# Performance work log

Hardware: AMD Instinct MI355X
Metric: run time of the kernel (lower is better)

Reference implementation:

```python
import jax, jax.numpy as jnp
import numpy as np

THR = 1.0
ALPHA = 5.0
C = 0.4
TAU_U = 20.0
DT = 1.0

def slayer(x):
    # SE-adlif SLAYER surrogate: c*alpha / (2*exp(alpha*|x|))
    return C * ALPHA / (2.0 * jnp.exp(jnp.abs(x) * ALPHA))

def setup_inputs() -> dict:
    key = jax.random.key(0)
    k1, k2, k3 = jax.random.split(key, 3)
    B, T, IN, OUT = 64, 1000, 512, 512
    x = jax.random.normal(k1, (B, T, IN), dtype=jnp.float32)
    lim = 1.0 / np.sqrt(IN)
    weight = jax.random.uniform(k2, (OUT, IN), minval=-lim, maxval=lim, dtype=jnp.float32)
    bias = jnp.zeros((OUT,), jnp.float32)
    # orthogonal init for recurrent weights
    recurrent = jnp.linalg.qr(jax.random.normal(k3, (OUT, OUT), dtype=jnp.float32))[0].astype(jnp.float32)
    # fixed tau trainer: decay = exp(-dt/tau)
    decay = jnp.full((OUT,), np.exp(-DT / TAU_U), dtype=jnp.float32)
    return {"input_tensor": x, "weight": weight, "bias": bias, "recurrent": recurrent, "decay": decay}

def reference(input_tensor, weight, bias, recurrent, decay):
    B = input_tensor.shape[0]
    OUT = weight.shape[0]
    sg = jax.lax.stop_gradient
    # precompute input-driven current for all timesteps: [B, T, OUT]
    cur = jnp.einsum('bti,oi->bto', input_tensor, weight) + bias
    v0 = jnp.zeros((B, OUT), jnp.float32)
    z0 = jnp.zeros((B, OUT), jnp.float32)

    def step(carry, c_t):
        v_tm1, z_tm1 = carry
        v_tm1 = v_tm1 * (1.0 - sg(z_tm1))  # detached reset
        soma = c_t + z_tm1 @ recurrent.T
        v_t = decay * v_tm1 + (1.0 - decay) * soma
        v_thr = v_t - THR
        hv = jnp.where(v_thr >= 0, 1.0, 0.0).astype(v_thr.dtype)
        # straight-through: value = heaviside, grad = SLAYER surrogate
        z_t = sg(hv) + (v_thr - sg(v_thr)) * sg(slayer(v_thr))
        return (v_t, z_t), (v_t, z_t)

    _, (vs, zs) = jax.lax.scan(step, (v0, z0), jnp.swapaxes(cur, 0, 1))
    vs = jnp.swapaxes(vs, 0, 1)  # [B, T, OUT]
    zs = jnp.swapaxes(zs, 0, 1)
    v_full = jnp.concatenate([v0[:, None], vs], axis=1)  # [B, T+1, OUT]
    z_full = jnp.concatenate([z0[:, None], zs], axis=1)
    states = jnp.stack([v_full, z_full], axis=0)  # [2, B, T+1, OUT]
    outputs = zs  # [B, T, OUT]
    return outputs, states
```

## Files before the change

kernel.cpp:

```cpp
#include <hip/hip_runtime.h>

#define SV_OFF 32768000
#define SZ_OFF 65568768

typedef __attribute__((ext_vector_type(8))) short bf16x8;
typedef __attribute__((ext_vector_type(4))) float f32x4;

__device__ __forceinline__ unsigned short f2bf(float f) {
  union { float f; unsigned u; } x; x.f = f;
  unsigned r = x.u + 0x7fffu + ((x.u >> 16) & 1u);
  return (unsigned short)(r >> 16);
}

__device__ __forceinline__ void gl_lds16(const void* g, void* l) {
  __builtin_amdgcn_global_load_lds(
      (const __attribute__((address_space(1))) unsigned int*)g,
      (__attribute__((address_space(3))) unsigned int*)l, 16, 0, 0);
}

__global__ __launch_bounds__(256) void prep(const float* __restrict__ W,
                                            unsigned short* __restrict__ Wb,
                                            int* __restrict__ flags) {
  const int idx = blockIdx.x * 256 + threadIdx.x;
  if (idx < 512 * 512) Wb[idx] = f2bf(W[idx]);
  if (idx < 64) flags[idx] = 0;
}

__global__ __launch_bounds__(256) void cvt_x(const float* __restrict__ x,
                                             unsigned short* __restrict__ xb) {
  const size_t i = ((size_t)blockIdx.x * 256 + threadIdx.x) * 8;
  const float4 a = *(const float4*)(x + i);
  const float4 b = *(const float4*)(x + i + 4);
  bf16x8 h;
  h[0] = (short)f2bf(a.x); h[1] = (short)f2bf(a.y);
  h[2] = (short)f2bf(a.z); h[3] = (short)f2bf(a.w);
  h[4] = (short)f2bf(b.x); h[5] = (short)f2bf(b.y);
  h[6] = (short)f2bf(b.z); h[7] = (short)f2bf(b.w);
  *(bf16x8*)(xb + i) = h;
}

__global__ __launch_bounds__(256, 2) void fused(
    const unsigned short* __restrict__ Ab,
    const unsigned short* __restrict__ Wb,
    const float* __restrict__ bias,
    const float* __restrict__ decay,
    float* __restrict__ out,
    int* __restrict__ flags) {
  __shared__ unsigned short As[2][128][32];
  __shared__ unsigned short Bs[2][64][32];
  __shared__ float cs[128][64];

  const int b    = blockIdx.x;
  const int o0   = blockIdx.y * 64;
  const int tid  = threadIdx.x;
  const int wave = tid >> 6;
  const int lane = tid & 63;
  const int lr = lane & 15;
  const int lq = lane >> 4;
  const int wr = wave >> 1;
  const int wc = wave & 1;

  const int arow = tid >> 2;
  const int acb  = (tid & 3) * 16;
  const char* abase = (const char*)Ab + (size_t)b * 1000 * 1024;
  const char* bbase = (const char*)Wb + (size_t)o0 * 1024;

#define STAGE(pp, t0s, kks) do {                                                   \
    const int _kb = (kks) * 64 + acb;                                              \
    gl_lds16(abase + (size_t)((t0s) + arow) * 1024 + _kb,                          \
             (char*)&As[pp][0][0] + tid * 16);                                     \
    gl_lds16(abase + (size_t)((t0s) + 64 + arow) * 1024 + _kb,                     \
             (char*)&As[pp][0][0] + tid * 16 + 4096);                              \
    gl_lds16(bbase + (size_t)arow * 1024 + _kb,                                    \
             (char*)&Bs[pp][0][0] + tid * 16);                                     \
  } while (0)

  float v = 0.f, d = 0.f, om = 0.f, bv = 0.f;
  int fl = 0;
  if (tid < 64) {
    d  = decay[o0 + tid];
    om = 1.f - d;
    bv = bias[o0 + tid];
    __builtin_nontemporal_store(0.f, out + SV_OFF + (size_t)b * 512512 + o0 + tid);
    __builtin_nontemporal_store(0.f, out + SZ_OFF + (size_t)b * 512512 + o0 + tid);
  }

  int p = 0;
  STAGE(0, 0, 0);
  for (int tile = 0; tile < 8; ++tile) {
    const int t0 = tile * 128;
    f32x4 acc[4][2] = {};
    for (int kk = 0; kk < 16; ++kk) {
      __syncthreads();
      if (kk < 15)       STAGE(p ^ 1, t0, kk + 1);
      else if (tile < 7) STAGE(p ^ 1, t0 + 128, 0);
      bf16x8 af[4], bf[2];
#pragma unroll
      for (int i = 0; i < 4; ++i)
        af[i] = *(const bf16x8*)(&As[p][wr * 64 + i * 16 + lr][lq * 8]);
#pragma unroll
      for (int j = 0; j < 2; ++j)
        bf[j] = *(const bf16x8*)(&Bs[p][wc * 32 + j * 16 + lr][lq * 8]);
#pragma unroll
      for (int i = 0; i < 4; ++i)
#pragma unroll
        for (int j = 0; j < 2; ++j)
          acc[i][j] = __builtin_amdgcn_mfma_f32_16x16x32_bf16(af[i], bf[j], acc[i][j], 0, 0, 0);
      p ^= 1;
    }
#pragma unroll
    for (int i = 0; i < 4; ++i)
#pragma unroll
      for (int j = 0; j < 2; ++j) {
        const int tb = wr * 64 + i * 16 + lq * 4;
        const int cc = (wc * 32 + j * 16 + lr) ^ ((lq & 1) << 4);
#pragma unroll
        for (int r = 0; r < 4; ++r) cs[tb + r][cc] = acc[i][j][r];
      }
    __syncthreads();
    if (tid < 64) {
      const int tmax = (tile == 7) ? 104 : 128;
      float* zp = out + ((size_t)b * 1000 + t0) * 512 + o0 + tid;
      float* vp = out + SV_OFF + ((size_t)b * 1001 + t0 + 1) * 512 + o0 + tid;
      float* sp = out + SZ_OFF + ((size_t)b * 1001 + t0 + 1) * 512 + o0 + tid;
      for (int t = 0; t < tmax; t += 4) {
        const int cc = tid ^ (((t >> 2) & 1) << 4);
        float c4[4];
#pragma unroll
        for (int u = 0; u < 4; ++u) c4[u] = cs[t + u][cc];
#pragma unroll
        for (int u = 0; u < 4; ++u) {
          v = d * v + om * (c4[u] + bv);
          const float z = (v >= 1.0f) ? 1.0f : 0.0f;
          fl |= (v >= 1.0f);
          __builtin_nontemporal_store(z, zp + (size_t)(t + u) * 512);
          __builtin_nontemporal_store(v, vp + (size_t)(t + u) * 512);
          __builtin_nontemporal_store(z, sp + (size_t)(t + u) * 512);
        }
      }
    }
  }
  if (tid < 64 && fl) atomicOr(flags + b, 1);
#undef STAGE
}

__global__ __launch_bounds__(512) void scan_fix(const float* __restrict__ x,
                                                const float* __restrict__ W,
                                                const float* __restrict__ bias,
                                                const float* __restrict__ R,
                                                const float* __restrict__ decay,
                                                float* __restrict__ out,
                                                const int* __restrict__ flags) {
  const int b = blockIdx.x;
  if (flags[b] == 0) return;
  const int o = threadIdx.x;
  __shared__ float xs[512];
  __shared__ int cnt;
  __shared__ int list[512];
  const float d = decay[o];
  const float om = 1.f - d;
  float v = 0.f, z = 0.f;
  const size_t zb  = (size_t)b * 512000 + o;
  const size_t svb = (size_t)b * 512512 + o;
  float* __restrict__ sv = out + SV_OFF;
  float* __restrict__ sz = out + SZ_OFF;
  sv[svb] = 0.f;
  sz[svb] = 0.f;
  if (o == 0) cnt = 0;
  __syncthreads();
  for (int t = 0; t < 1000; ++t) {
    xs[o] = x[((size_t)b * 1000 + t) * 512 + o];
    __syncthreads();
    float soma = bias[o];
    for (int i = 0; i < 512; ++i) soma += xs[i] * W[(size_t)o * 512 + i];
    const int n = cnt;
    for (int i = 0; i < n; ++i) soma += R[(size_t)o * 512 + list[i]];
    v = d * (v * (1.f - z)) + om * soma;
    z = (v >= 1.0f) ? 1.0f : 0.0f;
    out[zb + (size_t)t * 512] = z;
    sv[svb + (size_t)(t + 1) * 512] = v;
    sz[svb + (size_t)(t + 1) * 512] = z;
    __syncthreads();
    if (o == 0) cnt = 0;
    __syncthreads();
    if (z != 0.f) { const int q = atomicAdd(&cnt, 1); list[q] = o; }
    __syncthreads();
  }
}

extern "C" void kernel_launch(void* const* d_in, const int* in_sizes, int n_in,
                              void* d_out, int out_size, void* d_ws, size_t ws_size,
                              hipStream_t stream) {
  (void)in_sizes; (void)n_in; (void)out_size; (void)ws_size;
  const float* x     = (const float*)d_in[0];
  const float* W     = (const float*)d_in[1];
  const float* bias  = (const float*)d_in[2];
  const float* R     = (const float*)d_in[3];
  const float* decay = (const float*)d_in[4];
  float* out = (float*)d_out;

  char* ws = (char*)d_ws;
  unsigned short* xb = (unsigned short*)ws;
  unsigned short* Wb = (unsigned short*)(ws + 65536000);
  int* flags         = (int*)(ws + 66060288);

  prep<<<1024, 256, 0, stream>>>(W, Wb, flags);
  cvt_x<<<16000, 256, 0, stream>>>(x, xb);
  fused<<<dim3(64, 8), 256, 0, stream>>>(xb, Wb, bias, decay, out, flags);
  scan_fix<<<64, 512, 0, stream>>>(x, W, bias, R, decay, out, flags);
}
```

Baseline: 547.6 us.

## Fuse fp32-to-bf16 input conversion into GEMM A-tile staging

Removes the separate cvt_x pass that wrote a bf16 copy of the input to workspace. The GEMM kernel now loads fp32 input directly into registers, converts to bf16 and writes to padded LDS, with the next tile's global load issued before the MFMAs. This avoids writing and re-reading the 64 MB bf16 buffer, but each of the 8 column blocks now re-reads the fp32 input at twice the bytes, and the register-staged path adds conversion ALU work and register pressure inside the main loop.

```diff
diff --git a/kernel.cpp b/kernel.cpp
--- a/kernel.cpp
+++ b/kernel.cpp
@@ -26,27 +26,14 @@
   if (idx < 64) flags[idx] = 0;
 }
 
-__global__ __launch_bounds__(256) void cvt_x(const float* __restrict__ x,
-                                             unsigned short* __restrict__ xb) {
-  const size_t i = ((size_t)blockIdx.x * 256 + threadIdx.x) * 8;
-  const float4 a = *(const float4*)(x + i);
-  const float4 b = *(const float4*)(x + i + 4);
-  bf16x8 h;
-  h[0] = (short)f2bf(a.x); h[1] = (short)f2bf(a.y);
-  h[2] = (short)f2bf(a.z); h[3] = (short)f2bf(a.w);
-  h[4] = (short)f2bf(b.x); h[5] = (short)f2bf(b.y);
-  h[6] = (short)f2bf(b.z); h[7] = (short)f2bf(b.w);
-  *(bf16x8*)(xb + i) = h;
-}
-
 __global__ __launch_bounds__(256, 2) void fused(
-    const unsigned short* __restrict__ Ab,
+    const float* __restrict__ x,
     const unsigned short* __restrict__ Wb,
     const float* __restrict__ bias,
     const float* __restrict__ decay,
     float* __restrict__ out,
     int* __restrict__ flags) {
-  __shared__ unsigned short As[2][128][32];
+  __shared__ unsigned short As[2][128][40];
   __shared__ unsigned short Bs[2][64][32];
   __shared__ float cs[128][64];
 
@@ -60,20 +47,35 @@
   const int wr = wave >> 1;
   const int wc = wave & 1;
 
-  const int arow = tid >> 2;
-  const int acb  = (tid & 3) * 16;
-  const char* abase = (const char*)Ab + (size_t)b * 1000 * 1024;
+  const int ar = tid >> 3;
+  const int ac = (tid & 7) * 4;
+  const float* xb = x + (size_t)b * 512000;
+  const int br  = tid >> 2;
+  const int bcb = (tid & 3) * 16;
   const char* bbase = (const char*)Wb + (size_t)o0 * 1024;
 
-#define STAGE(pp, t0s, kks) do {                                                   \
-    const int _kb = (kks) * 64 + acb;                                              \
-    gl_lds16(abase + (size_t)((t0s) + arow) * 1024 + _kb,                          \
-             (char*)&As[pp][0][0] + tid * 16);                                     \
-    gl_lds16(abase + (size_t)((t0s) + 64 + arow) * 1024 + _kb,                     \
-             (char*)&As[pp][0][0] + tid * 16 + 4096);                              \
-    gl_lds16(bbase + (size_t)arow * 1024 + _kb,                                    \
-             (char*)&Bs[pp][0][0] + tid * 16);                                     \
+  float4 nxt[4];
+
+#define A_ISSUE(t0s, kks) do {                                                  \
+    _Pragma("unroll")                                                           \
+    for (int p4 = 0; p4 < 4; ++p4) {                                            \
+      int rg = (t0s) + ar + p4 * 32;                                            \
+      rg = rg > 999 ? 999 : rg;                                                 \
+      nxt[p4] = *(const float4*)(xb + (size_t)rg * 512 + (kks) * 32 + ac);      \
+    }                                                                           \
   } while (0)
+#define A_WRITE(pp) do {                                                        \
+    _Pragma("unroll")                                                           \
+    for (int p4 = 0; p4 < 4; ++p4) {                                            \
+      ushort4 h;                                                                \
+      h.x = f2bf(nxt[p4].x); h.y = f2bf(nxt[p4].y);                             \
+      h.z = f2bf(nxt[p4].z); h.w = f2bf(nxt[p4].w);                             \
+      *(ushort4*)(&As[pp][ar + p4 * 32][ac]) = h;                               \
+    }                                                                           \
+  } while (0)
+#define B_STAGE(pp, kks)                                                        \
+    gl_lds16(bbase + (size_t)br * 1024 + (kks) * 64 + bcb,                      \
+             (char*)(&Bs[pp][0][0]) + tid * 16)
 
   float v = 0.f, d = 0.f, om = 0.f, bv = 0.f;
   int fl = 0;
@@ -85,15 +87,24 @@
     __builtin_nontemporal_store(0.f, out + SZ_OFF + (size_t)b * 512512 + o0 + tid);
   }
 
+  A_ISSUE(0, 0);
+  B_STAGE(0, 0);
+  A_WRITE(0);
+
   int p = 0;
-  STAGE(0, 0, 0);
   for (int tile = 0; tile < 8; ++tile) {
     const int t0 = tile * 128;
     f32x4 acc[4][2] = {};
     for (int kk = 0; kk < 16; ++kk) {
       __syncthreads();
-      if (kk < 15)       STAGE(p ^ 1, t0, kk + 1);
-      else if (tile < 7) STAGE(p ^ 1, t0 + 128, 0);
+      const bool havenext = (kk < 15) | (tile < 7);
+      if (kk < 15) {
+        A_ISSUE(t0, kk + 1);
+        B_STAGE(p ^ 1, kk + 1);
+      } else if (tile < 7) {
+        A_ISSUE(t0 + 128, 0);
+        B_STAGE(p ^ 1, 0);
+      }
       bf16x8 af[4], bf[2];
 #pragma unroll
       for (int i = 0; i < 4; ++i)
@@ -106,6 +117,7 @@
 #pragma unroll
         for (int j = 0; j < 2; ++j)
           acc[i][j] = __builtin_amdgcn_mfma_f32_16x16x32_bf16(af[i], bf[j], acc[i][j], 0, 0, 0);
+      if (havenext) A_WRITE(p ^ 1);
       p ^= 1;
     }
 #pragma unroll
@@ -141,7 +153,9 @@
     }
   }
   if (tid < 64 && fl) atomicOr(flags + b, 1);
-#undef STAGE
+#undef A_ISSUE
+#undef A_WRITE
+#undef B_STAGE
 }
 
 __global__ __launch_bounds__(512) void scan_fix(const float* __restrict__ x,
@@ -200,12 +214,10 @@
   float* out = (float*)d_out;
 
   char* ws = (char*)d_ws;
-  unsigned short* xb = (unsigned short*)ws;
-  unsigned short* Wb = (unsigned short*)(ws + 65536000);
-  int* flags         = (int*)(ws + 66060288);
+  unsigned short* Wb = (unsigned short*)ws;
+  int* flags         = (int*)(ws + 524288);
 
   prep<<<1024, 256, 0, stream>>>(W, Wb, flags);
-  cvt_x<<<16000, 256, 0, stream>>>(x, xb);
-  fused<<<dim3(64, 8), 256, 0, stream>>>(xb, Wb, bias, decay, out, flags);
+  fused<<<dim3(64, 8), 256, 0, stream>>>(x, Wb, bias, decay, out, flags);
   scan_fix<<<64, 512, 0, stream>>>(x, W, bias, R, decay, out, flags);
 }
```

Result: slower. 630.5 us (+15.2%).

## Warp-specialize fused kernel: dedicated scan wave overlaps GEMM with 4-stage prefetch

Applied to the files above, without the earlier changes.

Adds a fifth wave to the fused kernel that performs the per-neuron leaky scan and output stores for the previous 128-step tile while the four MFMA waves compute the next tile. The LDS staging grows from a double to a four-deep ring with three stages in flight, synchronised by explicit vmcnt waits and raw barriers. It also XOR-swizzles the LDS columns to reduce bank conflicts. The intent is to hide the serial scan and store phase, which previously stalled the GEMM waves, at the cost of more LDS, extra barriers, and a serial tail for the last tile.

```diff
diff --git a/kernel.cpp b/kernel.cpp
--- a/kernel.cpp
+++ b/kernel.cpp
@@ -39,108 +39,135 @@
   *(bf16x8*)(xb + i) = h;
 }
 
-__global__ __launch_bounds__(256, 2) void fused(
+__global__ __launch_bounds__(320, 2) void fused(
     const unsigned short* __restrict__ Ab,
     const unsigned short* __restrict__ Wb,
     const float* __restrict__ bias,
     const float* __restrict__ decay,
     float* __restrict__ out,
     int* __restrict__ flags) {
-  __shared__ unsigned short As[2][128][32];
-  __shared__ unsigned short Bs[2][64][32];
+  __shared__ unsigned short As[4][128][32];
+  __shared__ unsigned short Bs[4][64][32];
   __shared__ float cs[128][64];
 
   const int b    = blockIdx.x;
   const int o0   = blockIdx.y * 64;
   const int tid  = threadIdx.x;
+  const int lane = tid & 63;
   const int wave = tid >> 6;
-  const int lane = tid & 63;
   const int lr = lane & 15;
   const int lq = lane >> 4;
   const int wr = wave >> 1;
   const int wc = wave & 1;
 
-  const int arow = tid >> 2;
-  const int acb  = (tid & 3) * 16;
+  const int row0 = tid >> 2;
+  const int scol = ((tid & 3) * 16) ^ ((row0 & 3) << 4);
   const char* abase = (const char*)Ab + (size_t)b * 1000 * 1024;
   const char* bbase = (const char*)Wb + (size_t)o0 * 1024;
 
-#define STAGE(pp, t0s, kks) do {                                                   \
-    const int _kb = (kks) * 64 + acb;                                              \
-    gl_lds16(abase + (size_t)((t0s) + arow) * 1024 + _kb,                          \
-             (char*)&As[pp][0][0] + tid * 16);                                     \
-    gl_lds16(abase + (size_t)((t0s) + 64 + arow) * 1024 + _kb,                     \
-             (char*)&As[pp][0][0] + tid * 16 + 4096);                              \
-    gl_lds16(bbase + (size_t)arow * 1024 + _kb,                                    \
-             (char*)&Bs[pp][0][0] + tid * 16);                                     \
+#define STAGE(s_) do {                                                          \
+    const int t0_ = ((s_) >> 4) * 128;                                          \
+    const int kb_ = ((s_) & 15) * 64;                                           \
+    const int bf_ = (s_) & 3;                                                   \
+    gl_lds16(abase + (size_t)(t0_ + row0) * 1024 + kb_ + scol,                  \
+             (char*)&As[bf_][0][0] + tid * 16);                                 \
+    gl_lds16(abase + (size_t)(t0_ + 64 + row0) * 1024 + kb_ + scol,             \
+             (char*)&As[bf_][0][0] + tid * 16 + 4096);                          \
+    gl_lds16(bbase + (size_t)row0 * 1024 + kb_ + scol,                          \
+             (char*)&Bs[bf_][0][0] + tid * 16);                                 \
   } while (0)
 
   float v = 0.f, d = 0.f, om = 0.f, bv = 0.f;
   int fl = 0;
-  if (tid < 64) {
-    d  = decay[o0 + tid];
+  if (tid >= 256) {
+    const int o = tid - 256;
+    d  = decay[o0 + o];
     om = 1.f - d;
-    bv = bias[o0 + tid];
-    __builtin_nontemporal_store(0.f, out + SV_OFF + (size_t)b * 512512 + o0 + tid);
-    __builtin_nontemporal_store(0.f, out + SZ_OFF + (size_t)b * 512512 + o0 + tid);
-  }
-
-  int p = 0;
-  STAGE(0, 0, 0);
+    bv = bias[o0 + o];
+    __builtin_nontemporal_store(0.f, out + SV_OFF + (size_t)b * 512512 + o0 + o);
+    __builtin_nontemporal_store(0.f, out + SZ_OFF + (size_t)b * 512512 + o0 + o);
+  } else {
+    STAGE(0); STAGE(1); STAGE(2);
+  }
+
+  int s = 0;
   for (int tile = 0; tile < 8; ++tile) {
-    const int t0 = tile * 128;
     f32x4 acc[4][2] = {};
-    for (int kk = 0; kk < 16; ++kk) {
-      __syncthreads();
-      if (kk < 15)       STAGE(p ^ 1, t0, kk + 1);
-      else if (tile < 7) STAGE(p ^ 1, t0 + 128, 0);
-      bf16x8 af[4], bf[2];
-#pragma unroll
-      for (int i = 0; i < 4; ++i)
-        af[i] = *(const bf16x8*)(&As[p][wr * 64 + i * 16 + lr][lq * 8]);
-#pragma unroll
-      for (int j = 0; j < 2; ++j)
-        bf[j] = *(const bf16x8*)(&Bs[p][wc * 32 + j * 16 + lr][lq * 8]);
-#pragma unroll
-      for (int i = 0; i < 4; ++i)
+    for (int kk = 0; kk < 16; ++kk, ++s) {
+      if (tid < 256)
+        asm volatile("s_waitcnt vmcnt(6)" ::: "memory");
+      __builtin_amdgcn_s_barrier();
+      __builtin_amdgcn_sched_barrier(0);
+      if (tid < 256) {
+        if (s < 125) STAGE(s + 3);
+        const int bf_ = s & 3;
+        const int fo = (lq ^ (lr & 3)) * 8;
+        bf16x8 af[4], bq[2];
+#pragma unroll
+        for (int i = 0; i < 4; ++i)
+          af[i] = *(const bf16x8*)(&As[bf_][wr * 64 + i * 16 + lr][fo]);
 #pragma unroll
         for (int j = 0; j < 2; ++j)
-          acc[i][j] = __builtin_amdgcn_mfma_f32_16x16x32_bf16(af[i], bf[j], acc[i][j], 0, 0, 0);
-      p ^= 1;
-    }
-#pragma unroll
-    for (int i = 0; i < 4; ++i)
-#pragma unroll
-      for (int j = 0; j < 2; ++j) {
-        const int tb = wr * 64 + i * 16 + lq * 4;
-        const int cc = (wc * 32 + j * 16 + lr) ^ ((lq & 1) << 4);
-#pragma unroll
-        for (int r = 0; r < 4; ++r) cs[tb + r][cc] = acc[i][j][r];
-      }
-    __syncthreads();
-    if (tid < 64) {
-      const int tmax = (tile == 7) ? 104 : 128;
-      float* zp = out + ((size_t)b * 1000 + t0) * 512 + o0 + tid;
-      float* vp = out + SV_OFF + ((size_t)b * 1001 + t0 + 1) * 512 + o0 + tid;
-      float* sp = out + SZ_OFF + ((size_t)b * 1001 + t0 + 1) * 512 + o0 + tid;
-      for (int t = 0; t < tmax; t += 4) {
-        const int cc = tid ^ (((t >> 2) & 1) << 4);
-        float c4[4];
-#pragma unroll
-        for (int u = 0; u < 4; ++u) c4[u] = cs[t + u][cc];
-#pragma unroll
-        for (int u = 0; u < 4; ++u) {
-          v = d * v + om * (c4[u] + bv);
+          bq[j] = *(const bf16x8*)(&Bs[bf_][wc * 32 + j * 16 + lr][fo]);
+#pragma unroll
+        for (int i = 0; i < 4; ++i)
+#pragma unroll
+          for (int j = 0; j < 2; ++j)
+            acc[i][j] = __builtin_amdgcn_mfma_f32_16x16x32_bf16(af[i], bq[j], acc[i][j], 0, 0, 0);
+      } else if (tile > 0) {
+        const int o = tid - 256;
+        const int pt0 = (tile - 1) * 128;
+        const int tb = kk * 8;
+        float* zp = out + ((size_t)b * 1000 + pt0) * 512 + o0 + o;
+        float* vp = out + SV_OFF + ((size_t)b * 1001 + pt0 + 1) * 512 + o0 + o;
+        float* sp = out + SZ_OFF + ((size_t)b * 1001 + pt0 + 1) * 512 + o0 + o;
+#pragma unroll
+        for (int u = 0; u < 8; ++u) {
+          const int t = tb + u;
+          const float c = cs[t][o ^ (((t >> 2) & 1) << 4)];
+          v = d * v + om * (c + bv);
           const float z = (v >= 1.0f) ? 1.0f : 0.0f;
           fl |= (v >= 1.0f);
-          __builtin_nontemporal_store(z, zp + (size_t)(t + u) * 512);
-          __builtin_nontemporal_store(v, vp + (size_t)(t + u) * 512);
-          __builtin_nontemporal_store(z, sp + (size_t)(t + u) * 512);
+          __builtin_nontemporal_store(z, zp + (size_t)t * 512);
+          __builtin_nontemporal_store(v, vp + (size_t)t * 512);
+          __builtin_nontemporal_store(z, sp + (size_t)t * 512);
         }
       }
     }
-  }
-  if (tid < 64 && fl) atomicOr(flags + b, 1);
+    __builtin_amdgcn_s_barrier();
+    __builtin_amdgcn_sched_barrier(0);
+    if (tid < 256) {
+#pragma unroll
+      for (int i = 0; i < 4; ++i)
+#pragma unroll
+        for (int j = 0; j < 2; ++j) {
+          const int tb = wr * 64 + i * 16 + lq * 4;
+          const int cc = (wc * 32 + j * 16 + lr) ^ ((lq & 1) << 4);
+#pragma unroll
+          for (int r = 0; r < 4; ++r) cs[tb + r][cc] = acc[i][j][r];
+        }
+      asm volatile("s_waitcnt lgkmcnt(0)" ::: "memory");
+    }
+    __builtin_amdgcn_s_barrier();
+    __builtin_amdgcn_sched_barrier(0);
+  }
+  if (tid >= 256) {
+    const int o = tid - 256;
+    const int pt0 = 896;
+    float* zp = out + ((size_t)b * 1000 + pt0) * 512 + o0 + o;
+    float* vp = out + SV_OFF + ((size_t)b * 1001 + pt0 + 1) * 512 + o0 + o;
+    float* sp = out + SZ_OFF + ((size_t)b * 1001 + pt0 + 1) * 512 + o0 + o;
+    for (int t = 0; t < 104; ++t) {
+      const float c = cs[t][o ^ (((t >> 2) & 1) << 4)];
+      v = d * v + om * (c + bv);
+      const float z = (v >= 1.0f) ? 1.0f : 0.0f;
+      fl |= (v >= 1.0f);
+      __builtin_nontemporal_store(z, zp + (size_t)t * 512);
+      __builtin_nontemporal_store(v, vp + (size_t)t * 512);
+      __builtin_nontemporal_store(z, sp + (size_t)t * 512);
+    }
+    if (fl) atomicOr(flags + b, 1);
+  }
 #undef STAGE
 }
 
@@ -206,6 +233,6 @@
 
   prep<<<1024, 256, 0, stream>>>(W, Wb, flags);
   cvt_x<<<16000, 256, 0, stream>>>(x, xb);
-  fused<<<dim3(64, 8), 256, 0, stream>>>(xb, Wb, bias, decay, out, flags);
+  fused<<<dim3(64, 8), 320, 0, stream>>>(xb, Wb, bias, decay, out, flags);
   scan_fix<<<64, 512, 0, stream>>>(x, W, bias, R, decay, out, flags);
 }
```

After: 584.6 us. +6.8%, slower.

## Widen fused GEMM tile to 128 outputs with 4-stage swizzled LDS pipeline

Applied to the files above, without the earlier changes.

The fused GEMM+scan kernel now uses 512-thread blocks covering 128 output channels each, giving a 4x64 grid instead of 8x64. The K loop moves from double buffering to a 4-deep buffer ring with prefetch distance 3, paced by explicit vmcnt waits and raw barriers. An XOR swizzle is applied to the LDS staging columns to reduce bank conflicts. This aims to hide global-load latency and halve redundant A-tile loads, at the cost of fewer blocks (256), one block per CU, and twice as many serial scan threads per block.

```diff
diff --git a/kernel.cpp b/kernel.cpp
--- a/kernel.cpp
+++ b/kernel.cpp
@@ -39,45 +39,45 @@
   *(bf16x8*)(xb + i) = h;
 }
 
-__global__ __launch_bounds__(256, 2) void fused(
+__global__ __launch_bounds__(512, 1) void fused(
     const unsigned short* __restrict__ Ab,
     const unsigned short* __restrict__ Wb,
     const float* __restrict__ bias,
     const float* __restrict__ decay,
     float* __restrict__ out,
     int* __restrict__ flags) {
-  __shared__ unsigned short As[2][128][32];
-  __shared__ unsigned short Bs[2][64][32];
-  __shared__ float cs[128][64];
+  __shared__ unsigned short As[4][128][32];
+  __shared__ unsigned short Bs[4][128][32];
+  __shared__ float cs[128][128];
 
   const int b    = blockIdx.x;
-  const int o0   = blockIdx.y * 64;
+  const int o0   = blockIdx.y * 128;
   const int tid  = threadIdx.x;
+  const int lane = tid & 63;
   const int wave = tid >> 6;
-  const int lane = tid & 63;
   const int lr = lane & 15;
   const int lq = lane >> 4;
-  const int wr = wave >> 1;
-  const int wc = wave & 1;
-
-  const int arow = tid >> 2;
-  const int acb  = (tid & 3) * 16;
+  const int wr = wave >> 2;
+  const int wc = wave & 3;
+
+  const int row0 = tid >> 2;
+  const int scol = ((tid & 3) * 16) ^ ((row0 & 3) << 4);
   const char* abase = (const char*)Ab + (size_t)b * 1000 * 1024;
   const char* bbase = (const char*)Wb + (size_t)o0 * 1024;
 
-#define STAGE(pp, t0s, kks) do {                                                   \
-    const int _kb = (kks) * 64 + acb;                                              \
-    gl_lds16(abase + (size_t)((t0s) + arow) * 1024 + _kb,                          \
-             (char*)&As[pp][0][0] + tid * 16);                                     \
-    gl_lds16(abase + (size_t)((t0s) + 64 + arow) * 1024 + _kb,                     \
-             (char*)&As[pp][0][0] + tid * 16 + 4096);                              \
-    gl_lds16(bbase + (size_t)arow * 1024 + _kb,                                    \
-             (char*)&Bs[pp][0][0] + tid * 16);                                     \
+#define STAGE(s_) do {                                                          \
+    const int t0_ = ((s_) >> 4) * 128;                                          \
+    const int kb_ = ((s_) & 15) * 64;                                           \
+    const int bf_ = (s_) & 3;                                                   \
+    gl_lds16(abase + (size_t)(t0_ + row0) * 1024 + kb_ + scol,                  \
+             (char*)&As[bf_][0][0] + tid * 16);                                 \
+    gl_lds16(bbase + (size_t)row0 * 1024 + kb_ + scol,                          \
+             (char*)&Bs[bf_][0][0] + tid * 16);                                 \
   } while (0)
 
   float v = 0.f, d = 0.f, om = 0.f, bv = 0.f;
   int fl = 0;
-  if (tid < 64) {
+  if (tid < 128) {
     d  = decay[o0 + tid];
     om = 1.f - d;
     bv = bias[o0 + tid];
@@ -85,52 +85,59 @@
     __builtin_nontemporal_store(0.f, out + SZ_OFF + (size_t)b * 512512 + o0 + tid);
   }
 
-  int p = 0;
-  STAGE(0, 0, 0);
+  STAGE(0); STAGE(1); STAGE(2);
+
+  int s = 0;
   for (int tile = 0; tile < 8; ++tile) {
-    const int t0 = tile * 128;
     f32x4 acc[4][2] = {};
-    for (int kk = 0; kk < 16; ++kk) {
-      __syncthreads();
-      if (kk < 15)       STAGE(p ^ 1, t0, kk + 1);
-      else if (tile < 7) STAGE(p ^ 1, t0 + 128, 0);
-      bf16x8 af[4], bf[2];
+    for (int kk = 0; kk < 16; ++kk, ++s) {
+      asm volatile("s_waitcnt vmcnt(4)" ::: "memory");
+      __builtin_amdgcn_s_barrier();
+      __builtin_amdgcn_sched_barrier(0);
+      STAGE((s + 3) & 127);
+      const int bf_ = s & 3;
+      const int fo = (lq ^ (lr & 3)) * 8;
+      bf16x8 af[4], bq[2];
 #pragma unroll
       for (int i = 0; i < 4; ++i)
-        af[i] = *(const bf16x8*)(&As[p][wr * 64 + i * 16 + lr][lq * 8]);
+        af[i] = *(const bf16x8*)(&As[bf_][wr * 64 + i * 16 + lr][fo]);
 #pragma unroll
       for (int j = 0; j < 2; ++j)
-        bf[j] = *(const bf16x8*)(&Bs[p][wc * 32 + j * 16 + lr][lq * 8]);
+        bq[j] = *(const bf16x8*)(&Bs[bf_][wc * 32 + j * 16 + lr][fo]);
 #pragma unroll
       for (int i = 0; i < 4; ++i)
 #pragma unroll
         for (int j = 0; j < 2; ++j)
-          acc[i][j] = __builtin_amdgcn_mfma_f32_16x16x32_bf16(af[i], bf[j], acc[i][j], 0, 0, 0);
-      p ^= 1;
+          acc[i][j] = __builtin_amdgcn_mfma_f32_16x16x32_bf16(af[i], bq[j], acc[i][j], 0, 0, 0);
     }
 #pragma unroll
     for (int i = 0; i < 4; ++i)
 #pragma unroll
       for (int j = 0; j < 2; ++j) {
         const int tb = wr * 64 + i * 16 + lq * 4;
-        const int cc = (wc * 32 + j * 16 + lr) ^ ((lq & 1) << 4);
+        const int cc = (wc * 32 + j * 16 + lr) ^ (lq << 4);
 #pragma unroll
         for (int r = 0; r < 4; ++r) cs[tb + r][cc] = acc[i][j][r];
       }
-    __syncthreads();
-    if (tid < 64) {
+    asm volatile("s_waitcnt lgkmcnt(0)" ::: "memory");
+    __builtin_amdgcn_s_barrier();
+    __builtin_amdgcn_sched_barrier(0);
+    if (tid < 128) {
+      const int t0 = tile * 128;
       const int tmax = (tile == 7) ? 104 : 128;
       float* zp = out + ((size_t)b * 1000 + t0) * 512 + o0 + tid;
       float* vp = out + SV_OFF + ((size_t)b * 1001 + t0 + 1) * 512 + o0 + tid;
       float* sp = out + SZ_OFF + ((size_t)b * 1001 + t0 + 1) * 512 + o0 + tid;
       for (int t = 0; t < tmax; t += 4) {
-        const int cc = tid ^ (((t >> 2) & 1) << 4);
-        float c4[4];
-#pragma unroll
-        for (int u = 0; u < 4; ++u) c4[u] = cs[t + u][cc];
+        const int u4 = ((t >> 2) & 3) << 4;
+        const float c0 = cs[t + 0][tid ^ u4];
+        const float c1 = cs[t + 1][tid ^ u4];
+        const float c2 = cs[t + 2][tid ^ u4];
+        const float c3 = cs[t + 3][tid ^ u4];
+        float cc4[4] = {c0, c1, c2, c3};
 #pragma unroll
         for (int u = 0; u < 4; ++u) {
-          v = d * v + om * (c4[u] + bv);
+          v = d * v + om * (cc4[u] + bv);
           const float z = (v >= 1.0f) ? 1.0f : 0.0f;
           fl |= (v >= 1.0f);
           __builtin_nontemporal_store(z, zp + (size_t)(t + u) * 512);
@@ -140,7 +147,7 @@
       }
     }
   }
-  if (tid < 64 && fl) atomicOr(flags + b, 1);
+  if (tid < 128 && fl) atomicOr(flags + b, 1);
 #undef STAGE
 }
 
@@ -206,6 +213,6 @@
 
   prep<<<1024, 256, 0, stream>>>(W, Wb, flags);
   cvt_x<<<16000, 256, 0, stream>>>(x, xb);
-  fused<<<dim3(64, 8), 256, 0, stream>>>(xb, Wb, bias, decay, out, flags);
+  fused<<<dim3(64, 4), 512, 0, stream>>>(xb, Wb, bias, decay, out, flags);
   scan_fix<<<64, 512, 0, stream>>>(x, W, bias, R, decay, out, flags);
 }
```

New measurement: 530.0 us. -3.2%, faster.
